# Kernel tuning notes

Measured on AMD Instinct MI355X. Metric: run time of the kernel, lower is better.

The kernel has to match this reference:

```python
import jax, jax.numpy as jnp
import numpy as np

VALID_DIM = 20
NUM_FEATURES = 100000
EMB_DIM = 64
ATT_DIM = 32
B = 8192


def setup_inputs() -> dict:
    key = jax.random.key(0)
    ks = jax.random.split(key, 8)
    features = jax.random.randint(ks[0], (B, VALID_DIM), 0, NUM_FEATURES)
    feature_values = jax.random.uniform(ks[1], (B, VALID_DIM), dtype=jnp.float32)
    emb_table = jax.random.normal(ks[2], (NUM_FEATURES, EMB_DIM), dtype=jnp.float32) * 0.01
    bias_table = jnp.zeros((NUM_FEATURES, 1), dtype=jnp.float32)
    global_bias = jnp.zeros((1,), dtype=jnp.float32)
    att_w1 = jax.random.normal(ks[3], (ATT_DIM, EMB_DIM), dtype=jnp.float32) * (1.0 / np.sqrt(EMB_DIM))
    att_b1 = jnp.zeros((ATT_DIM,), dtype=jnp.float32)
    att_w2 = jax.random.normal(ks[4], (ATT_DIM,), dtype=jnp.float32)
    pred_w = jnp.ones((EMB_DIM,), dtype=jnp.float32)
    return {
        "features": features,
        "feature_values": feature_values,
        "emb_table": emb_table,
        "bias_table": bias_table,
        "global_bias": global_bias,
        "att_w1": att_w1,
        "att_b1": att_b1,
        "att_w2": att_w2,
        "pred_w": pred_w,
    }


def reference(features, feature_values, emb_table, bias_table, global_bias,
              att_w1, att_b1, att_w2, pred_w):
    # gather + scale embeddings: [B, F, D]
    e = emb_table[features] * feature_values[..., None]
    # pairwise elementwise products over upper-triangular field pairs: [B, P, D]
    ii, jj = jnp.triu_indices(VALID_DIM, k=1)
    ele = e[:, ii, :] * e[:, jj, :]
    # attention MLP: Linear->ReLU->Linear(no bias)->softmax over pairs
    h = jax.nn.relu(jnp.einsum('bpd,ad->bpa', ele, att_w1) + att_b1)
    logits = jnp.einsum('bpa,a->bp', h, att_w2)
    att = jax.nn.softmax(logits, axis=1)
    afm = jnp.einsum('bp,bpd->bd', att, ele)  # weighted sum over pairs
    pred = jnp.einsum('bd,d->b', afm, pred_w)
    fb = (bias_table[features][..., 0] * feature_values).sum(axis=1)
    return pred + fb + global_bias[0]
```

## Files before the change

kernel.cpp:

```cpp
#include <hip/hip_runtime.h>

#define VDIM 20
#define NPAIR 190
#define NT 12
#define EMB 64
#define ERS2 72

typedef __attribute__((ext_vector_type(8))) _Float16 f16x8;
typedef __attribute__((ext_vector_type(4))) _Float16 f16x4;
typedef __attribute__((ext_vector_type(4))) float    f32x4;

__device__ __forceinline__ f16x8 pack8(f32x4 a, f32x4 b) {
    auto p0 = __builtin_amdgcn_cvt_pkrtz(a[0], a[1]);
    auto p1 = __builtin_amdgcn_cvt_pkrtz(a[2], a[3]);
    auto p2 = __builtin_amdgcn_cvt_pkrtz(b[0], b[1]);
    auto p3 = __builtin_amdgcn_cvt_pkrtz(b[2], b[3]);
    f16x8 r;
    r[0] = p0[0]; r[1] = p0[1]; r[2] = p1[0]; r[3] = p1[1];
    r[4] = p2[0]; r[5] = p2[1]; r[6] = p3[0]; r[7] = p3[1];
    return r;
}

__global__ __launch_bounds__(256, 4)
void afm_fwd(const int* __restrict__ feats, const float* __restrict__ fvals,
             const float* __restrict__ emb, const float* __restrict__ btab,
             const float* __restrict__ gbias, const float* __restrict__ w1,
             const float* __restrict__ b1, const float* __restrict__ w2,
             const float* __restrict__ pw, float* __restrict__ out, int B)
{
    __shared__ __align__(16) _Float16 ls_e[4][VDIM * ERS2];

    const int tid  = threadIdx.x;
    const int wv   = tid >> 6;
    const int lane = tid & 63;
    const int g    = lane >> 4;
    const int a0   = lane & 15;
    const int b    = blockIdx.x * 4 + wv;
    if (b >= B) return;

    int ff = 0; float vv = 0.f;
    if (lane < VDIM) { ff = feats[b * VDIM + lane]; vv = fvals[b * VDIM + lane]; }

    f16x8 aw[2][2];
    #pragma unroll
    for (int mta = 0; mta < 2; ++mta)
        #pragma unroll
        for (int ks = 0; ks < 2; ++ks) {
            const f32x4* wp = reinterpret_cast<const f32x4*>(
                                  w1 + (a0 + 16*mta) * EMB + ks*32 + g*8);
            aw[mta][ks] = pack8(wp[0], wp[1]);
        }
    f16x8 apw[2];
    {
        const f16x8 zz = {};
        #pragma unroll
        for (int ks = 0; ks < 2; ++ks) {
            const f32x4* pp = reinterpret_cast<const f32x4*>(pw + ks*32 + g*8);
            apw[ks] = (a0 == 0) ? pack8(pp[0], pp[1]) : zz;
        }
    }

    f32x4 b1v[2], w2v[2];
    #pragma unroll
    for (int mta = 0; mta < 2; ++mta) {
        b1v[mta] = *reinterpret_cast<const f32x4*>(b1 + mta*16 + g*4);
        w2v[mta] = *reinterpret_cast<const f32x4*>(w2 + mta*16 + g*4);
    }

    float fbv = (lane < VDIM) ? btab[ff] * vv : 0.f;
    #pragma unroll
    for (int off = 32; off; off >>= 1) fbv += __shfl_xor(fbv, off);
    const float gbv = gbias[0];

    _Float16* ew = ls_e[wv];
    #pragma unroll
    for (int q = 0; q < 5; ++q) {
        int   row = q * 4 + g;
        int   fI  = __shfl(ff, row);
        float vI  = __shfl(vv, row);
        f32x4 ev  = reinterpret_cast<const f32x4*>(emb + (size_t)fI * EMB)[a0];
        auto h0 = __builtin_amdgcn_cvt_pkrtz(ev[0] * vI, ev[1] * vI);
        auto h1 = __builtin_amdgcn_cvt_pkrtz(ev[2] * vI, ev[3] * vI);
        f16x4 hv;
        hv[0] = h0[0]; hv[1] = h0[1]; hv[2] = h1[0]; hv[3] = h1[1];
        *reinterpret_cast<f16x4*>(
            reinterpret_cast<char*>(ew) + row * (ERS2*2) + a0 * 8) = hv;
    }
    asm volatile("s_waitcnt lgkmcnt(0)" ::: "memory");
    __builtin_amdgcn_wave_barrier();

    float num = 0.f, den = 0.f;
    #pragma unroll 2
    for (int nt = 0; nt < NT; ++nt) {
        int p = nt * 16 + a0;
        bool valid = p < NPAIR;
        if (!valid) p = 0;
        int i = (int)((39.0f - sqrtf((float)(1521 - 8 * p))) * 0.5f);
        int t  = (i * (39 - i)) >> 1;
        int t1 = ((i + 1) * (38 - i)) >> 1;
        if (p < t)        { --i; t = (i * (39 - i)) >> 1; }
        else if (p >= t1) { ++i; t = t1; }
        int j = p - t + i + 1;

        const char* bi = reinterpret_cast<const char*>(ew) + i * (ERS2*2);
        const char* bj = reinterpret_cast<const char*>(ew) + j * (ERS2*2);

        f32x4 acc0 = b1v[0];
        f32x4 acc1 = b1v[1];
        f32x4 accs = (f32x4){0.f, 0.f, 0.f, 0.f};
        #pragma unroll
        for (int ks = 0; ks < 2; ++ks) {
            f16x8 ei = *reinterpret_cast<const f16x8*>(bi + ks*64 + g*16);
            f16x8 ej = *reinterpret_cast<const f16x8*>(bj + ks*64 + g*16);
            f16x8 pr = ei * ej;
            acc0 = __builtin_amdgcn_mfma_f32_16x16x32_f16(aw[0][ks], pr, acc0, 0, 0, 0);
            acc1 = __builtin_amdgcn_mfma_f32_16x16x32_f16(aw[1][ks], pr, acc1, 0, 0, 0);
            accs = __builtin_amdgcn_mfma_f32_16x16x32_f16(apw[ks],   pr, accs, 0, 0, 0);
        }
        float tl = 0.f;
        #pragma unroll
        for (int r = 0; r < 4; ++r) {
            tl += fmaxf(acc0[r], 0.f) * w2v[0][r];
            tl += fmaxf(acc1[r], 0.f) * w2v[1][r];
        }
        tl += __shfl_xor(tl, 16);
        tl += __shfl_xor(tl, 32);
        float w = valid ? __expf(tl) : 0.f;
        num = fmaf(w, accs[0], num);
        den += w;
    }

    num += __shfl_xor(num, 1);  den += __shfl_xor(den, 1);
    num += __shfl_xor(num, 2);  den += __shfl_xor(den, 2);
    num += __shfl_xor(num, 4);  den += __shfl_xor(den, 4);
    num += __shfl_xor(num, 8);  den += __shfl_xor(den, 8);

    if (lane == 0)
        out[b] = num / den + fbv + gbv;
}

extern "C" void kernel_launch(void* const* d_in, const int* in_sizes, int n_in,
                              void* d_out, int out_size, void* d_ws, size_t ws_size,
                              hipStream_t stream)
{
    const int*   feats = (const int*)  d_in[0];
    const float* fvals = (const float*)d_in[1];
    const float* emb   = (const float*)d_in[2];
    const float* btab  = (const float*)d_in[3];
    const float* gb    = (const float*)d_in[4];
    const float* w1    = (const float*)d_in[5];
    const float* b1    = (const float*)d_in[6];
    const float* w2    = (const float*)d_in[7];
    const float* pw    = (const float*)d_in[8];
    float*       out   = (float*)d_out;

    const int B = in_sizes[0] / VDIM;
    afm_fwd<<<(B + 3) / 4, 256, 0, stream>>>(feats, fvals, emb, btab, gb,
                                             w1, b1, w2, pw, out, B);
}
```

Baseline: 29.15 us.

## Process two batch rows per wavefront to amortize weight setup and index math

```diff
diff --git a/kernel.cpp b/kernel.cpp
--- a/kernel.cpp
+++ b/kernel.cpp
@@ -28,18 +28,22 @@
              const float* __restrict__ b1, const float* __restrict__ w2,
              const float* __restrict__ pw, float* __restrict__ out, int B)
 {
-    __shared__ __align__(16) _Float16 ls_e[4][VDIM * ERS2];
+    __shared__ __align__(16) _Float16 ls_e[8][VDIM * ERS2];
 
     const int tid  = threadIdx.x;
     const int wv   = tid >> 6;
     const int lane = tid & 63;
     const int g    = lane >> 4;
     const int a0   = lane & 15;
-    const int b    = blockIdx.x * 4 + wv;
-    if (b >= B) return;
+    const int b0   = blockIdx.x * 8 + wv * 2;
+    const int b1s  = b0 + 1;
+    if (b0 >= B) return;
 
     int ff = 0; float vv = 0.f;
-    if (lane < VDIM) { ff = feats[b * VDIM + lane]; vv = fvals[b * VDIM + lane]; }
+    {
+        int r = lane & 31, s = lane >> 5, sb = b0 + s;
+        if (r < VDIM && sb < B) { ff = feats[sb * VDIM + r]; vv = fvals[sb * VDIM + r]; }
+    }
 
     f16x8 aw[2][2];
     #pragma unroll
@@ -67,30 +71,34 @@
         w2v[mta] = *reinterpret_cast<const f32x4*>(w2 + mta*16 + g*4);
     }
 
-    float fbv = (lane < VDIM) ? btab[ff] * vv : 0.f;
+    float fbv = ((lane & 31) < VDIM) ? btab[ff] * vv : 0.f;
     #pragma unroll
-    for (int off = 32; off; off >>= 1) fbv += __shfl_xor(fbv, off);
+    for (int off = 16; off; off >>= 1) fbv += __shfl_xor(fbv, off);
     const float gbv = gbias[0];
 
-    _Float16* ew = ls_e[wv];
+    _Float16* ew0 = ls_e[wv * 2];
+    _Float16* ew1 = ls_e[wv * 2 + 1];
     #pragma unroll
     for (int q = 0; q < 5; ++q) {
         int   row = q * 4 + g;
-        int   fI  = __shfl(ff, row);
-        float vI  = __shfl(vv, row);
-        f32x4 ev  = reinterpret_cast<const f32x4*>(emb + (size_t)fI * EMB)[a0];
-        auto h0 = __builtin_amdgcn_cvt_pkrtz(ev[0] * vI, ev[1] * vI);
-        auto h1 = __builtin_amdgcn_cvt_pkrtz(ev[2] * vI, ev[3] * vI);
-        f16x4 hv;
-        hv[0] = h0[0]; hv[1] = h0[1]; hv[2] = h1[0]; hv[3] = h1[1];
-        *reinterpret_cast<f16x4*>(
-            reinterpret_cast<char*>(ew) + row * (ERS2*2) + a0 * 8) = hv;
+        int   fI0 = __shfl(ff, row);        float vI0 = __shfl(vv, row);
+        int   fI1 = __shfl(ff, 32 + row);   float vI1 = __shfl(vv, 32 + row);
+        f32x4 ev0 = reinterpret_cast<const f32x4*>(emb + (size_t)fI0 * EMB)[a0];
+        f32x4 ev1 = reinterpret_cast<const f32x4*>(emb + (size_t)fI1 * EMB)[a0];
+        auto h00 = __builtin_amdgcn_cvt_pkrtz(ev0[0] * vI0, ev0[1] * vI0);
+        auto h01 = __builtin_amdgcn_cvt_pkrtz(ev0[2] * vI0, ev0[3] * vI0);
+        auto h10 = __builtin_amdgcn_cvt_pkrtz(ev1[0] * vI1, ev1[1] * vI1);
+        auto h11 = __builtin_amdgcn_cvt_pkrtz(ev1[2] * vI1, ev1[3] * vI1);
+        f16x4 hv0; hv0[0]=h00[0]; hv0[1]=h00[1]; hv0[2]=h01[0]; hv0[3]=h01[1];
+        f16x4 hv1; hv1[0]=h10[0]; hv1[1]=h10[1]; hv1[2]=h11[0]; hv1[3]=h11[1];
+        *reinterpret_cast<f16x4*>(reinterpret_cast<char*>(ew0) + row*(ERS2*2) + a0*8) = hv0;
+        *reinterpret_cast<f16x4*>(reinterpret_cast<char*>(ew1) + row*(ERS2*2) + a0*8) = hv1;
     }
     asm volatile("s_waitcnt lgkmcnt(0)" ::: "memory");
     __builtin_amdgcn_wave_barrier();
 
-    float num = 0.f, den = 0.f;
-    #pragma unroll 2
+    float num0 = 0.f, den0 = 0.f, num1 = 0.f, den1 = 0.f;
+    #pragma unroll 1
     for (int nt = 0; nt < NT; ++nt) {
         int p = nt * 16 + a0;
         bool valid = p < NPAIR;
@@ -101,42 +109,53 @@
         if (p < t)        { --i; t = (i * (39 - i)) >> 1; }
         else if (p >= t1) { ++i; t = t1; }
         int j = p - t + i + 1;
+        const int oi = i * (ERS2 * 2), oj = j * (ERS2 * 2);
 
-        const char* bi = reinterpret_cast<const char*>(ew) + i * (ERS2*2);
-        const char* bj = reinterpret_cast<const char*>(ew) + j * (ERS2*2);
-
-        f32x4 acc0 = b1v[0];
-        f32x4 acc1 = b1v[1];
-        f32x4 accs = (f32x4){0.f, 0.f, 0.f, 0.f};
+        f32x4 acc00 = b1v[0], acc01 = b1v[1], accs0 = (f32x4){0.f,0.f,0.f,0.f};
+        f32x4 acc10 = b1v[0], acc11 = b1v[1], accs1 = (f32x4){0.f,0.f,0.f,0.f};
         #pragma unroll
         for (int ks = 0; ks < 2; ++ks) {
-            f16x8 ei = *reinterpret_cast<const f16x8*>(bi + ks*64 + g*16);
-            f16x8 ej = *reinterpret_cast<const f16x8*>(bj + ks*64 + g*16);
-            f16x8 pr = ei * ej;
-            acc0 = __builtin_amdgcn_mfma_f32_16x16x32_f16(aw[0][ks], pr, acc0, 0, 0, 0);
-            acc1 = __builtin_amdgcn_mfma_f32_16x16x32_f16(aw[1][ks], pr, acc1, 0, 0, 0);
-            accs = __builtin_amdgcn_mfma_f32_16x16x32_f16(apw[ks],   pr, accs, 0, 0, 0);
+            const char* c0 = reinterpret_cast<const char*>(ew0);
+            const char* c1 = reinterpret_cast<const char*>(ew1);
+            f16x8 ei0 = *reinterpret_cast<const f16x8*>(c0 + oi + ks*64 + g*16);
+            f16x8 ej0 = *reinterpret_cast<const f16x8*>(c0 + oj + ks*64 + g*16);
+            f16x8 ei1 = *reinterpret_cast<const f16x8*>(c1 + oi + ks*64 + g*16);
+            f16x8 ej1 = *reinterpret_cast<const f16x8*>(c1 + oj + ks*64 + g*16);
+            f16x8 pr0 = ei0 * ej0;
+            f16x8 pr1 = ei1 * ej1;
+            acc00 = __builtin_amdgcn_mfma_f32_16x16x32_f16(aw[0][ks], pr0, acc00, 0, 0, 0);
+            acc01 = __builtin_amdgcn_mfma_f32_16x16x32_f16(aw[1][ks], pr0, acc01, 0, 0, 0);
+            accs0 = __builtin_amdgcn_mfma_f32_16x16x32_f16(apw[ks],   pr0, accs0, 0, 0, 0);
+            acc10 = __builtin_amdgcn_mfma_f32_16x16x32_f16(aw[0][ks], pr1, acc10, 0, 0, 0);
+            acc11 = __builtin_amdgcn_mfma_f32_16x16x32_f16(aw[1][ks], pr1, acc11, 0, 0, 0);
+            accs1 = __builtin_amdgcn_mfma_f32_16x16x32_f16(apw[ks],   pr1, accs1, 0, 0, 0);
         }
-        float tl = 0.f;
+        float tl0 = 0.f, tl1 = 0.f;
         #pragma unroll
         for (int r = 0; r < 4; ++r) {
-            tl += fmaxf(acc0[r], 0.f) * w2v[0][r];
-            tl += fmaxf(acc1[r], 0.f) * w2v[1][r];
+            tl0 += fmaxf(acc00[r], 0.f) * w2v[0][r];
+            tl0 += fmaxf(acc01[r], 0.f) * w2v[1][r];
+            tl1 += fmaxf(acc10[r], 0.f) * w2v[0][r];
+            tl1 += fmaxf(acc11[r], 0.f) * w2v[1][r];
         }
-        tl += __shfl_xor(tl, 16);
-        tl += __shfl_xor(tl, 32);
-        float w = valid ? __expf(tl) : 0.f;
-        num = fmaf(w, accs[0], num);
-        den += w;
+        tl0 += __shfl_xor(tl0, 16);  tl1 += __shfl_xor(tl1, 16);
+        tl0 += __shfl_xor(tl0, 32);  tl1 += __shfl_xor(tl1, 32);
+        float w0 = valid ? __expf(tl0) : 0.f;
+        float w1x = valid ? __expf(tl1) : 0.f;
+        num0 = fmaf(w0,  accs0[0], num0);  den0 += w0;
+        num1 = fmaf(w1x, accs1[0], num1);  den1 += w1x;
     }
 
-    num += __shfl_xor(num, 1);  den += __shfl_xor(den, 1);
-    num += __shfl_xor(num, 2);  den += __shfl_xor(den, 2);
-    num += __shfl_xor(num, 4);  den += __shfl_xor(den, 4);
-    num += __shfl_xor(num, 8);  den += __shfl_xor(den, 8);
-
-    if (lane == 0)
-        out[b] = num / den + fbv + gbv;
+    #pragma unroll
+    for (int off = 8; off; off >>= 1) {
+        num0 += __shfl_xor(num0, off);  den0 += __shfl_xor(den0, off);
+        num1 += __shfl_xor(num1, off);  den1 += __shfl_xor(den1, off);
+    }
+    float fb1 = __shfl(fbv, 32);
+    if (lane == 0) {
+        out[b0] = num0 / den0 + fbv + gbv;
+        if (b1s < B) out[b1s] = num1 / den1 + fb1 + gbv;
+    }
 }
 
 extern "C" void kernel_launch(void* const* d_in, const int* in_sizes, int n_in,
@@ -155,6 +174,6 @@
     float*       out   = (float*)d_out;
 
     const int B = in_sizes[0] / VDIM;
-    afm_fwd<<<(B + 3) / 4, 256, 0, stream>>>(feats, fvals, emb, btab, gb,
+    afm_fwd<<<(B + 7) / 8, 256, 0, stream>>>(feats, fvals, emb, btab, gb,
                                              w1, b1, w2, pw, out, B);
 }
```

Result: faster. 28.35 us (-2.8%).

## Process four samples per wavefront to amortize pair-index math and weight loads

Applied to the files above, without the earlier changes.

```diff
diff --git a/kernel.cpp b/kernel.cpp
--- a/kernel.cpp
+++ b/kernel.cpp
@@ -5,6 +5,7 @@
 #define NT 12
 #define EMB 64
 #define ERS2 72
+#define SPW 4
 
 typedef __attribute__((ext_vector_type(8))) _Float16 f16x8;
 typedef __attribute__((ext_vector_type(4))) _Float16 f16x4;
@@ -21,25 +22,20 @@
     return r;
 }
 
-__global__ __launch_bounds__(256, 4)
+__global__ __launch_bounds__(64, 3)
 void afm_fwd(const int* __restrict__ feats, const float* __restrict__ fvals,
              const float* __restrict__ emb, const float* __restrict__ btab,
              const float* __restrict__ gbias, const float* __restrict__ w1,
              const float* __restrict__ b1, const float* __restrict__ w2,
              const float* __restrict__ pw, float* __restrict__ out, int B)
 {
-    __shared__ __align__(16) _Float16 ls_e[4][VDIM * ERS2];
+    __shared__ __align__(16) _Float16 ls_e[SPW][VDIM * ERS2];
 
-    const int tid  = threadIdx.x;
-    const int wv   = tid >> 6;
-    const int lane = tid & 63;
+    const int lane = threadIdx.x & 63;
     const int g    = lane >> 4;
     const int a0   = lane & 15;
-    const int b    = blockIdx.x * 4 + wv;
-    if (b >= B) return;
-
-    int ff = 0; float vv = 0.f;
-    if (lane < VDIM) { ff = feats[b * VDIM + lane]; vv = fvals[b * VDIM + lane]; }
+    const int b0   = blockIdx.x * SPW;
+    if (b0 >= B) return;
 
     f16x8 aw[2][2];
     #pragma unroll
@@ -67,30 +63,56 @@
         w2v[mta] = *reinterpret_cast<const f32x4*>(w2 + mta*16 + g*4);
     }
 
-    float fbv = (lane < VDIM) ? btab[ff] * vv : 0.f;
+    float fbv = 0.f;
+    {
+        int sb = b0 + g;
+        if (sb < B) {
+            int   f0 = feats[sb * VDIM + a0];
+            float v0 = fvals[sb * VDIM + a0];
+            fbv = btab[f0] * v0;
+            if (a0 < 4) {
+                int   f1 = feats[sb * VDIM + 16 + a0];
+                float v1 = fvals[sb * VDIM + 16 + a0];
+                fbv = fmaf(btab[f1], v1, fbv);
+            }
+        }
+        fbv += __shfl_xor(fbv, 1);
+        fbv += __shfl_xor(fbv, 2);
+        fbv += __shfl_xor(fbv, 4);
+        fbv += __shfl_xor(fbv, 8);
+    }
+    const float gbv = gbias[0];
+    float fbs0 = __shfl(fbv, 0),  fbs1 = __shfl(fbv, 16);
+    float fbs2 = __shfl(fbv, 32), fbs3 = __shfl(fbv, 48);
+
     #pragma unroll
-    for (int off = 32; off; off >>= 1) fbv += __shfl_xor(fbv, off);
-    const float gbv = gbias[0];
-
-    _Float16* ew = ls_e[wv];
-    #pragma unroll
-    for (int q = 0; q < 5; ++q) {
-        int   row = q * 4 + g;
-        int   fI  = __shfl(ff, row);
-        float vI  = __shfl(vv, row);
-        f32x4 ev  = reinterpret_cast<const f32x4*>(emb + (size_t)fI * EMB)[a0];
-        auto h0 = __builtin_amdgcn_cvt_pkrtz(ev[0] * vI, ev[1] * vI);
-        auto h1 = __builtin_amdgcn_cvt_pkrtz(ev[2] * vI, ev[3] * vI);
-        f16x4 hv;
-        hv[0] = h0[0]; hv[1] = h0[1]; hv[2] = h1[0]; hv[3] = h1[1];
-        *reinterpret_cast<f16x4*>(
-            reinterpret_cast<char*>(ew) + row * (ERS2*2) + a0 * 8) = hv;
+    for (int s = 0; s < SPW; ++s) {
+        int sb = b0 + s;
+        if (sb < B) {
+            _Float16* ew = ls_e[s];
+            #pragma unroll
+            for (int q = 0; q < 5; ++q) {
+                int   row = q * 4 + g;
+                int   fI  = feats[sb * VDIM + row];
+                float vI  = fvals[sb * VDIM + row];
+                f32x4 ev  = reinterpret_cast<const f32x4*>(emb + (size_t)fI * EMB)[a0];
+                auto h0 = __builtin_amdgcn_cvt_pkrtz(ev[0] * vI, ev[1] * vI);
+                auto h1 = __builtin_amdgcn_cvt_pkrtz(ev[2] * vI, ev[3] * vI);
+                f16x4 hv; hv[0]=h0[0]; hv[1]=h0[1]; hv[2]=h1[0]; hv[3]=h1[1];
+                *reinterpret_cast<f16x4*>(
+                    reinterpret_cast<char*>(ew) + row*(ERS2*2) + a0*8) = hv;
+            }
+        }
     }
     asm volatile("s_waitcnt lgkmcnt(0)" ::: "memory");
     __builtin_amdgcn_wave_barrier();
 
-    float num = 0.f, den = 0.f;
-    #pragma unroll 2
+    float num[SPW], den[SPW];
+    #pragma unroll
+    for (int s = 0; s < SPW; ++s) { num[s] = 0.f; den[s] = 0.f; }
+    const f32x4 z4 = (f32x4){0.f, 0.f, 0.f, 0.f};
+
+    #pragma unroll 1
     for (int nt = 0; nt < NT; ++nt) {
         int p = nt * 16 + a0;
         bool valid = p < NPAIR;
@@ -101,42 +123,56 @@
         if (p < t)        { --i; t = (i * (39 - i)) >> 1; }
         else if (p >= t1) { ++i; t = t1; }
         int j = p - t + i + 1;
+        const int oi = i * (ERS2 * 2), oj = j * (ERS2 * 2);
 
-        const char* bi = reinterpret_cast<const char*>(ew) + i * (ERS2*2);
-        const char* bj = reinterpret_cast<const char*>(ew) + j * (ERS2*2);
-
-        f32x4 acc0 = b1v[0];
-        f32x4 acc1 = b1v[1];
-        f32x4 accs = (f32x4){0.f, 0.f, 0.f, 0.f};
+        f32x4 acc0[SPW], acc1[SPW], accs[SPW];
+        #pragma unroll
+        for (int s = 0; s < SPW; ++s) {
+            acc0[s] = b1v[0]; acc1[s] = b1v[1]; accs[s] = z4;
+        }
         #pragma unroll
         for (int ks = 0; ks < 2; ++ks) {
-            f16x8 ei = *reinterpret_cast<const f16x8*>(bi + ks*64 + g*16);
-            f16x8 ej = *reinterpret_cast<const f16x8*>(bj + ks*64 + g*16);
-            f16x8 pr = ei * ej;
-            acc0 = __builtin_amdgcn_mfma_f32_16x16x32_f16(aw[0][ks], pr, acc0, 0, 0, 0);
-            acc1 = __builtin_amdgcn_mfma_f32_16x16x32_f16(aw[1][ks], pr, acc1, 0, 0, 0);
-            accs = __builtin_amdgcn_mfma_f32_16x16x32_f16(apw[ks],   pr, accs, 0, 0, 0);
+            #pragma unroll
+            for (int s = 0; s < SPW; ++s) {
+                const char* c = reinterpret_cast<const char*>(ls_e[s]);
+                f16x8 ei = *reinterpret_cast<const f16x8*>(c + oi + ks*64 + g*16);
+                f16x8 ej = *reinterpret_cast<const f16x8*>(c + oj + ks*64 + g*16);
+                f16x8 pr = ei * ej;
+                acc0[s] = __builtin_amdgcn_mfma_f32_16x16x32_f16(aw[0][ks], pr, acc0[s], 0, 0, 0);
+                acc1[s] = __builtin_amdgcn_mfma_f32_16x16x32_f16(aw[1][ks], pr, acc1[s], 0, 0, 0);
+                accs[s] = __builtin_amdgcn_mfma_f32_16x16x32_f16(apw[ks],   pr, accs[s], 0, 0, 0);
+            }
         }
-        float tl = 0.f;
         #pragma unroll
-        for (int r = 0; r < 4; ++r) {
-            tl += fmaxf(acc0[r], 0.f) * w2v[0][r];
-            tl += fmaxf(acc1[r], 0.f) * w2v[1][r];
+        for (int s = 0; s < SPW; ++s) {
+            float tl = 0.f;
+            #pragma unroll
+            for (int r = 0; r < 4; ++r) {
+                tl += fmaxf(acc0[s][r], 0.f) * w2v[0][r];
+                tl += fmaxf(acc1[s][r], 0.f) * w2v[1][r];
+            }
+            tl += __shfl_xor(tl, 16);
+            tl += __shfl_xor(tl, 32);
+            float w = valid ? __expf(tl) : 0.f;
+            num[s] = fmaf(w, accs[s][0], num[s]);
+            den[s] += w;
         }
-        tl += __shfl_xor(tl, 16);
-        tl += __shfl_xor(tl, 32);
-        float w = valid ? __expf(tl) : 0.f;
-        num = fmaf(w, accs[0], num);
-        den += w;
     }
 
-    num += __shfl_xor(num, 1);  den += __shfl_xor(den, 1);
-    num += __shfl_xor(num, 2);  den += __shfl_xor(den, 2);
-    num += __shfl_xor(num, 4);  den += __shfl_xor(den, 4);
-    num += __shfl_xor(num, 8);  den += __shfl_xor(den, 8);
-
-    if (lane == 0)
-        out[b] = num / den + fbv + gbv;
+    #pragma unroll
+    for (int s = 0; s < SPW; ++s) {
+        #pragma unroll
+        for (int off = 8; off; off >>= 1) {
+            num[s] += __shfl_xor(num[s], off);
+            den[s] += __shfl_xor(den[s], off);
+        }
+    }
+    if (lane == 0) {
+        float fb[SPW] = {fbs0, fbs1, fbs2, fbs3};
+        #pragma unroll
+        for (int s = 0; s < SPW; ++s)
+            if (b0 + s < B) out[b0 + s] = num[s] / den[s] + fb[s] + gbv;
+    }
 }
 
 extern "C" void kernel_launch(void* const* d_in, const int* in_sizes, int n_in,
@@ -155,6 +191,6 @@
     float*       out   = (float*)d_out;
 
     const int B = in_sizes[0] / VDIM;
-    afm_fwd<<<(B + 3) / 4, 256, 0, stream>>>(feats, fvals, emb, btab, gb,
-                                             w1, b1, w2, pw, out, B);
+    afm_fwd<<<(B + SPW - 1) / SPW, 64, 0, stream>>>(feats, fvals, emb, btab, gb,
+                                                    w1, b1, w2, pw, out, B);
 }
```

Result: slower. 30.75 us (+5.5%).
